# Performance work log

Measured on AMD Instinct MI355X. Metric: run time of the kernel, lower is better.

The kernel has to match this reference:

```python
import jax, jax.numpy as jnp
import numpy as np

N_STEPS = 64          # sample['N']
G = 1.0               # sample['g'] (constant diffusion)
NUM_SAMPLES = 2       # num_samples_per_obs
W_SCALE = 0.05

# interpolant coefficients: alpha(s)=1-s, beta(s)=s, sigma(s)=1-s
# derivatives: alpha_dot=-1, beta_dot=1, sigma_dot=-1

def b_net(x, x0, s, W1, b1, W2, b2, W3, b3):
    # B_net(interpolant, current_state, s): MLP on concat([x, x0, s])
    sf = jnp.full(x.shape[:-1] + (1,), s, dtype=x.dtype)
    inp = jnp.concatenate([x, x0, sf], axis=-1)      # [B, 2*dim+1]
    h = jax.nn.relu(inp @ W1 + b1)
    h = jax.nn.relu(h @ W2 + b2)
    return h @ W3 + b3                                # [B, dim]


def setup_inputs() -> dict:
    key = jax.random.key(0)
    ks = jax.random.split(key, 4)
    num_obs, dim, hid = 65536, 64, 256
    X0 = jax.random.normal(ks[0], (num_obs, dim), dtype=jnp.float32)
    W1 = jax.random.normal(ks[1], (2 * dim + 1, hid), dtype=jnp.float32) * W_SCALE
    W2 = jax.random.normal(ks[2], (hid, hid), dtype=jnp.float32) * W_SCALE
    W3 = jax.random.normal(ks[3], (hid, dim), dtype=jnp.float32) * W_SCALE
    return {
        "X0": X0,
        "W1": W1, "b1": jnp.zeros((hid,), jnp.float32),
        "W2": W2, "b2": jnp.zeros((hid,), jnp.float32),
        "W3": W3, "b3": jnp.zeros((dim,), jnp.float32),
    }


def reference(X0, W1, b1, W2, b2, W3, b3):
    time = jnp.linspace(0.0, 1.0, N_STEPS + 1, dtype=X0.dtype)
    ds = jnp.asarray(1.0 / N_STEPS, X0.dtype)
    sqrt_ds = jnp.sqrt(ds)
    params = (W1, b1, W2, b2, W3, b3)

    def sample_one(key):
        k0, kloop = jax.random.split(key)
        # first Euler step: X = X0 + ds*B(X0,X0,0) + sigma(0)*sqrt(ds)*eta
        eta0 = jax.random.normal(k0, X0.shape, X0.dtype)
        X = X0 + ds * b_net(X0, X0, time[0], *params) + (1.0 - time[0]) * sqrt_ds * eta0

        def step(carry, n):
            X, key = carry
            key, kn = jax.random.split(key)
            s = time[n]
            al, ald = 1.0 - s, -1.0
            bt, btd = s, 1.0
            sg, sgd = 1.0 - s, -1.0
            drift_b = b_net(X, X0, s, *params)
            # score correction (self.score)
            c = btd * X + (bt * ald - btd * al) * X0
            A = 1.0 / (s * sg * (btd * sg - bt * sgd))
            score = A * (bt * drift_b - c)
            # adjusted drift: drift + 0.5*(g^2 - sigma^2)*score
            control = 0.5 * (G ** 2 - sg ** 2) * score
            eta = jax.random.normal(kn, X.shape, X.dtype)
            X = X + ds * (drift_b + control) + G * sqrt_ds * eta
            return (X, key), None

        (X, _), _ = jax.lax.scan(step, (X, kloop), jnp.arange(1, N_STEPS))
        return X

    keys = jax.random.split(jax.random.key(1), NUM_SAMPLES)
    samples = jax.vmap(sample_one)(keys)   # [num_samples, num_obs, dim]
    return samples
```

## Files before the change

kernel.cpp:

```cpp
#include <hip/hip_runtime.h>
#include <stdint.h>


#define PARTITIONABLE 1

namespace {

constexpr int   kObs    = 65536;
constexpr int   kDim    = 64;
constexpr int   kSteps  = 64;
constexpr float kDs     = 1.0f / 64.0f;
constexpr float kSqrtDs = 0.125f;

constexpr int kWeightBytes = 256 * 1024;
constexpr int kKeysOff     = kWeightBytes;
constexpr int kStabOff     = kKeysOff + 1024;

typedef _Float16 f16x8 __attribute__((ext_vector_type(8)));
typedef _Float16 f16x4 __attribute__((ext_vector_type(4)));
typedef float    f32x4 __attribute__((ext_vector_type(4)));

#define MFMA16(a, b, c) __builtin_amdgcn_mfma_f32_16x16x32_f16((a), (b), (c), 0, 0, 0)

__device__ __forceinline__ uint32_t rotl(uint32_t v, int r) {
  return (v << r) | (v >> (32 - r));
}

__device__ __forceinline__ void tf2x32(uint32_t k0, uint32_t k1,
                                       uint32_t& x0, uint32_t& x1) {
  uint32_t k2 = k0 ^ k1 ^ 0x1BD11BDAu;
  x0 += k0; x1 += k1;
  x0 += x1; x1 = rotl(x1, 13); x1 ^= x0;
  x0 += x1; x1 = rotl(x1, 15); x1 ^= x0;
  x0 += x1; x1 = rotl(x1, 26); x1 ^= x0;
  x0 += x1; x1 = rotl(x1,  6); x1 ^= x0;
  x0 += k1; x1 += k2 + 1u;
  x0 += x1; x1 = rotl(x1, 17); x1 ^= x0;
  x0 += x1; x1 = rotl(x1, 29); x1 ^= x0;
  x0 += x1; x1 = rotl(x1, 16); x1 ^= x0;
  x0 += x1; x1 = rotl(x1, 24); x1 ^= x0;
  x0 += k2; x1 += k0 + 2u;
  x0 += x1; x1 = rotl(x1, 13); x1 ^= x0;
  x0 += x1; x1 = rotl(x1, 15); x1 ^= x0;
  x0 += x1; x1 = rotl(x1, 26); x1 ^= x0;
  x0 += x1; x1 = rotl(x1,  6); x1 ^= x0;
  x0 += k0; x1 += k1 + 3u;
  x0 += x1; x1 = rotl(x1, 17); x1 ^= x0;
  x0 += x1; x1 = rotl(x1, 29); x1 ^= x0;
  x0 += x1; x1 = rotl(x1, 16); x1 ^= x0;
  x0 += x1; x1 = rotl(x1, 24); x1 ^= x0;
  x0 += k1; x1 += k2 + 4u;
  x0 += x1; x1 = rotl(x1, 13); x1 ^= x0;
  x0 += x1; x1 = rotl(x1, 15); x1 ^= x0;
  x0 += x1; x1 = rotl(x1, 26); x1 ^= x0;
  x0 += x1; x1 = rotl(x1,  6); x1 ^= x0;
  x0 += k2; x1 += k0 + 5u;
}

__device__ __forceinline__ void jax_split(uint32_t k0, uint32_t k1,
                                          uint32_t& a0, uint32_t& a1,
                                          uint32_t& b0, uint32_t& b1) {
#if PARTITIONABLE
  uint32_t x0 = 0u, x1 = 0u; tf2x32(k0, k1, x0, x1); a0 = x0; a1 = x1;
  uint32_t y0 = 0u, y1 = 1u; tf2x32(k0, k1, y0, y1); b0 = y0; b1 = y1;
#else
  uint32_t x0 = 0u, x1 = 2u; tf2x32(k0, k1, x0, x1);
  uint32_t y0 = 1u, y1 = 3u; tf2x32(k0, k1, y0, y1);
  a0 = x0; a1 = y0; b0 = x1; b1 = y1;
#endif
}

__device__ __forceinline__ uint32_t draw_bits(uint32_t k0, uint32_t k1, uint32_t i) {
#if PARTITIONABLE
  uint32_t x0 = 0u, x1 = i;
  tf2x32(k0, k1, x0, x1);
  return x0 ^ x1;
#else
  const uint32_t half = (uint32_t)kObs * kDim / 2;
  if (i < half) {
    uint32_t x0 = i, x1 = i + half; tf2x32(k0, k1, x0, x1); return x0;
  } else {
    uint32_t x0 = i - half, x1 = i; tf2x32(k0, k1, x0, x1); return x1;
  }
#endif
}

__device__ __forceinline__ float erfinv32(float x) {
  float w = -__logf(fmaf(-x, x, 1.0f));
  float p;
  if (w < 5.0f) {
    w = w - 2.5f;
    p =            2.81022636e-08f;
    p = fmaf(p, w, 3.43273939e-07f);
    p = fmaf(p, w, -3.5233877e-06f);
    p = fmaf(p, w, -4.39150654e-06f);
    p = fmaf(p, w, 0.00021858087f);
    p = fmaf(p, w, -0.00125372503f);
    p = fmaf(p, w, -0.00417768164f);
    p = fmaf(p, w, 0.246640727f);
    p = fmaf(p, w, 1.50140941f);
  } else {
    w = sqrtf(w) - 3.0f;
    p =            -0.000200214257f;
    p = fmaf(p, w, 0.000100950558f);
    p = fmaf(p, w, 0.00134934322f);
    p = fmaf(p, w, -0.00367342844f);
    p = fmaf(p, w, 0.00573950773f);
    p = fmaf(p, w, -0.0076224613f);
    p = fmaf(p, w, 0.00943887047f);
    p = fmaf(p, w, 1.00167406f);
    p = fmaf(p, w, 2.83297682f);
  }
  return p * x;
}

__device__ __forceinline__ float bits_to_normal(uint32_t bits) {
  const float lo = -0.99999994f;
  float f = __uint_as_float(0x3f800000u | (bits >> 9)) - 1.0f;
  float u = fmaxf(lo, fmaf(f, 2.0f, lo));
  return 1.41421356237f * erfinv32(u);
}

}

__global__ void prep_weights(const float* __restrict__ W1,
                             const float* __restrict__ W2,
                             const float* __restrict__ W3,
                             _Float16* __restrict__ ws) {
  const int G = blockIdx.x;
  const int t = threadIdx.x;

  if (G >= 256) {
    if (t < 2) {
      uint32_t* kout = (uint32_t*)((char*)ws + kKeysOff) + t * 128;
      uint32_t s0a, s0b, s1a, s1b;
      jax_split(0u, 1u, s0a, s0b, s1a, s1b);
      const uint32_t sk0 = t ? s1a : s0a;
      const uint32_t sk1 = t ? s1b : s0b;
      uint32_t kd0, kd1, kl0, kl1;
      jax_split(sk0, sk1, kd0, kd1, kl0, kl1);
      kout[0] = kd0; kout[1] = kd1;
      for (int n = 1; n < kSteps; ++n) {
        uint32_t na, nb, xa, xb;
        jax_split(kl0, kl1, na, nb, xa, xb);
        kl0 = na; kl1 = nb;
        kout[2 * n] = xa; kout[2 * n + 1] = xb;
      }
    }
    if (t < kSteps) {
      const float s  = (float)t * kDs;
      const float sg = 1.0f - s;
      f32x4 v;
      v[0] = s;
      v[1] = (t == 0) ? 0.0f : 1.0f / (s * sg);
      v[2] = 0.5f * (1.0f - sg * sg);
      v[3] = kDs * v[2] * v[1];
      *(f32x4*)((char*)ws + kStabOff + t * 16) = v;
    }
    return;
  }

  const int lane = t >> 2;
  const int j0   = (t & 3) * 2;
  const int w    = G >> 5;
  const int T    = G & 31;
  const int lm   = lane & 15;
  const int kb   = (lane >> 4) << 3;

#pragma unroll
  for (int jj = 0; jj < 2; ++jj) {
    const int j = j0 + jj;
    float v;
    if (T < 8) {
      const int mt = T >> 2, kt = T & 3;
      const int col = w * 32 + mt * 16 + lm;
      const int k   = kt * 32 + kb + j;
      v = W1[k * 256 + col];
    } else if (T < 24) {
      const int u = T - 8;
      const int mt = u >> 3, kt = u & 7;
      const int col = w * 32 + mt * 16 + lm;
      const int k   = kt * 32 + kb + j;
      v = W2[k * 256 + col];
    } else {
      const int kt  = T - 24;
      const int col = (w >> 1) * 16 + lm;
      const int k   = kt * 32 + kb + j;
      v = W3[k * 64 + col];
    }
    ws[(size_t)G * 512 + lane * 8 + j] = (_Float16)v;
  }
}

__global__ __launch_bounds__(512, 2)
void sde_mfma(const float* __restrict__ X0g,
              const float* __restrict__ W1,
              const float* __restrict__ b1,
              const float* __restrict__ b2,
              const float* __restrict__ b3,
              const _Float16* __restrict__ ws,
              float* __restrict__ out) {
  __shared__ alignas(16) char  xAf [8 * 1024];
  __shared__ alignas(16) char  h1f [32 * 1024];
  __shared__ alignas(16) char  h2f [32 * 1024];
  __shared__ alignas(16) float bb  [832];

  const int t    = threadIdx.x;
  const int w    = t >> 6;
  const int l    = t & 63;
  const int lq   = l >> 4;
  const int lm   = l & 15;
  const int samp = blockIdx.x >> 10;
  const int tile = blockIdx.x & 1023;
  const int r0   = tile * 64;
  const int mt3  = w >> 1;
  const int ntb  = (w & 1) * 2;
  const int d0   = mt3 * 16 + lq * 4;

  const int rb  = l * 16;
  const int lo1 = ((lq >> 1) * 16 + lm) * 16 + (lq & 1) * 8;
  const int kt3 = mt3 >> 1;
  const int ln3 = (((mt3 & 1) * 2 + (lq >> 1)) * 16 + lm) * 16 + (lq & 1) * 8;

  if (t < 256) {
    bb[t]       = b1[t];
    bb[256 + t] = W1[128 * 256 + t];
    bb[512 + t] = b2[t];
  } else if (t < 320) {
    bb[768 + (t - 256)] = b3[t - 256];
  }

  {
    const int li = t >> 3;
    const int ci = (t & 7) * 8;
    const float* p = X0g + (size_t)(r0 + li) * kDim + ci;
    const float4 a = *(const float4*)p;
    const float4 b = *(const float4*)(p + 4);
    f16x8 h;
    h[0] = (_Float16)a.x; h[1] = (_Float16)a.y;
    h[2] = (_Float16)a.z; h[3] = (_Float16)a.w;
    h[4] = (_Float16)b.x; h[5] = (_Float16)b.y;
    h[6] = (_Float16)b.z; h[7] = (_Float16)b.w;
    const int fa = ((ci >> 5) * 4 + (li >> 4)) * 1024 +
                   (((ci >> 3) & 3) * 16 + (li & 15)) * 16;
    *(f16x8*)(xAf + fa) = h;
    *(f16x8*)(h1f + fa) = h;
  }

  float xv[2][4];
  f32x4 x0q[2];
#pragma unroll
  for (int ni = 0; ni < 2; ++ni) {
    const int row = (ntb + ni) * 16 + lm;
    x0q[ni] = *(const f32x4*)(X0g + (size_t)(r0 + row) * kDim + d0);
#pragma unroll
    for (int q = 0; q < 4; ++q) xv[ni][q] = x0q[ni][q];
  }
  const uint32_t giA = (uint32_t)((r0 + ntb * 16 + lm) * kDim + d0);
  const uint32_t giB = giA + 16u * kDim;

  const char* pW = (const char*)ws + (size_t)w * 32768 + l * 16;
  f16x8 wL1[2][2], wx0[2][2], wL2[16], wL3[8];
#pragma unroll
  for (int mt = 0; mt < 2; ++mt) {
    wL1[mt][0] = *(const f16x8*)(pW + (mt * 4 + 0) * 1024);
    wL1[mt][1] = *(const f16x8*)(pW + (mt * 4 + 1) * 1024);
    wx0[mt][0] = *(const f16x8*)(pW + (mt * 4 + 2) * 1024);
    wx0[mt][1] = *(const f16x8*)(pW + (mt * 4 + 3) * 1024);
  }
#pragma unroll
  for (int i = 0; i < 16; ++i) wL2[i] = *(const f16x8*)(pW + (8 + i) * 1024);
#pragma unroll
  for (int i = 0; i < 8; ++i)  wL3[i] = *(const f16x8*)(pW + (24 + i) * 1024);

  const uint32_t* keys = (const uint32_t*)((const char*)ws + kKeysOff) + samp * 128;
  const f32x4*    stab = (const f32x4*)((const char*)ws + kStabOff);

  __syncthreads();

  f16x4 pre[4][2];
#pragma unroll
  for (int nt = 0; nt < 4; ++nt) {
    const f16x8 xf0 = *(const f16x8*)(h1f + (0 * 4 + nt) * 1024 + rb);
    const f16x8 xf1 = *(const f16x8*)(h1f + (1 * 4 + nt) * 1024 + rb);
#pragma unroll
    for (int mt = 0; mt < 2; ++mt) {
      f32x4 p = {0.f, 0.f, 0.f, 0.f};
      p = MFMA16(wx0[mt][0], xf0, p);
      p = MFMA16(wx0[mt][1], xf1, p);
      f16x4 ph;
#pragma unroll
      for (int q = 0; q < 4; ++q) ph[q] = (_Float16)p[q];
      pre[nt][mt] = ph;
    }
  }
  __syncthreads();

  float etaA[4], etaB[4];
  {
    const uint32_t ka = keys[0], kb0 = keys[1];
#pragma unroll
    for (int q = 0; q < 4; ++q) etaA[q] = bits_to_normal(draw_bits(ka, kb0, giA + q));
#pragma unroll
    for (int q = 0; q < 4; ++q) etaB[q] = bits_to_normal(draw_bits(ka, kb0, giB + q));
  }

  for (int n = 0; n < kSteps; ++n) {
    const f32x4 st = stab[n];
    const float s = st[0], P = st[3];
    const int np = (n + 1 < kSteps) ? n + 1 : n;
    const uint32_t kna = keys[2 * np], knb = keys[2 * np + 1];

#pragma unroll
    for (int nt = 0; nt < 4; ++nt) {
      const f16x8 bf0 = *(const f16x8*)(xAf + (0 * 4 + nt) * 1024 + rb);
      const f16x8 bf1 = *(const f16x8*)(xAf + (1 * 4 + nt) * 1024 + rb);
#pragma unroll
      for (int mt = 0; mt < 2; ++mt) {
        f32x4 c = {0.f, 0.f, 0.f, 0.f};
        c = MFMA16(wL1[mt][0], bf0, c);
        c = MFMA16(wL1[mt][1], bf1, c);
        const int nb = w * 32 + mt * 16 + lq * 4;
        const f32x4 bq = *(const f32x4*)&bb[nb];
        const f32x4 wq = *(const f32x4*)&bb[256 + nb];
        const f16x4 ph = pre[nt][mt];
        f16x4 o;
#pragma unroll
        for (int q = 0; q < 4; ++q)
          o[q] = (_Float16)fmaxf(c[q] + (float)ph[q] + fmaf(s, wq[q], bq[q]), 0.f);
        *(f16x4*)(h1f + (w * 4 + nt) * 1024 + mt * 512 + lo1) = o;
      }
    }
    __syncthreads();

    float enA[4], enB[4];
#pragma unroll
    for (int ntp = 0; ntp < 2; ++ntp) {
      f32x4 c[2][2];
#pragma unroll
      for (int mt = 0; mt < 2; ++mt)
#pragma unroll
        for (int ni = 0; ni < 2; ++ni)
          c[mt][ni] = (f32x4){0.f, 0.f, 0.f, 0.f};
#pragma unroll
      for (int half = 0; half < 2; ++half) {
        f16x8 bh[2][4];
#pragma unroll
        for (int ni = 0; ni < 2; ++ni)
#pragma unroll
          for (int k4 = 0; k4 < 4; ++k4)
            bh[ni][k4] = *(const f16x8*)
                (h1f + ((half * 4 + k4) * 4 + ntp * 2 + ni) * 1024 + rb);
#pragma unroll
        for (int mt = 0; mt < 2; ++mt)
#pragma unroll
          for (int k4 = 0; k4 < 4; ++k4) {
            const f16x8 aW = wL2[mt * 8 + half * 4 + k4];
            c[mt][0] = MFMA16(aW, bh[0][k4], c[mt][0]);
            c[mt][1] = MFMA16(aW, bh[1][k4], c[mt][1]);
          }
      }
      if (ntp == 0) {
#pragma unroll
        for (int q = 0; q < 4; ++q)
          enA[q] = bits_to_normal(draw_bits(kna, knb, giA + q));
      } else {
#pragma unroll
        for (int q = 0; q < 4; ++q)
          enB[q] = bits_to_normal(draw_bits(kna, knb, giB + q));
      }
#pragma unroll
      for (int mt = 0; mt < 2; ++mt) {
        const int nb = w * 32 + mt * 16 + lq * 4;
        const f32x4 bq = *(const f32x4*)&bb[512 + nb];
#pragma unroll
        for (int ni = 0; ni < 2; ++ni) {
          f16x4 o;
#pragma unroll
          for (int q = 0; q < 4; ++q)
            o[q] = (_Float16)fmaxf(c[mt][ni][q] + bq[q], 0.f);
          *(f16x4*)(h2f + (w * 4 + ntp * 2 + ni) * 1024 + mt * 512 + lo1) = o;
        }
      }
    }
    __syncthreads();

    const f32x4 b3q = *(const f32x4*)&bb[768 + d0];
#pragma unroll
    for (int ni = 0; ni < 2; ++ni) {
      f32x4 dA = {0.f, 0.f, 0.f, 0.f}, dB = {0.f, 0.f, 0.f, 0.f};
#pragma unroll
      for (int half = 0; half < 2; ++half) {
        f16x8 bh[4];
#pragma unroll
        for (int k4 = 0; k4 < 4; ++k4)
          bh[k4] = *(const f16x8*)
              (h2f + ((half * 4 + k4) * 4 + ntb + ni) * 1024 + rb);
        dA = MFMA16(wL3[half * 4 + 0], bh[0], dA);
        dB = MFMA16(wL3[half * 4 + 1], bh[1], dB);
        dA = MFMA16(wL3[half * 4 + 2], bh[2], dA);
        dB = MFMA16(wL3[half * 4 + 3], bh[3], dB);
      }
      f16x4 hx;
#pragma unroll
      for (int q = 0; q < 4; ++q) {
        const float ov  = dA[q] + dB[q] + b3q[q];
        const float eta = ni ? etaB[q] : etaA[q];
        const float t1  = fmaf(s, ov, x0q[ni][q] - xv[ni][q]);
        float nx = fmaf(kSqrtDs, eta, xv[ni][q]);
        nx = fmaf(kDs, ov, nx);
        nx = fmaf(P, t1, nx);
        xv[ni][q] = nx;
        hx[q] = (_Float16)nx;
      }
      *(f16x4*)(xAf + (kt3 * 4 + ntb + ni) * 1024 + ln3) = hx;
    }
#pragma unroll
    for (int q = 0; q < 4; ++q) { etaA[q] = enA[q]; etaB[q] = enB[q]; }
    __syncthreads();
  }

#pragma unroll
  for (int ni = 0; ni < 2; ++ni) {
    const int row = (ntb + ni) * 16 + lm;
    const size_t ob = (size_t)samp * ((size_t)kObs * kDim) +
                      (size_t)(r0 + row) * kDim + d0;
    f32x4 v;
#pragma unroll
    for (int q = 0; q < 4; ++q) v[q] = xv[ni][q];
    *(f32x4*)(out + ob) = v;
  }
}

extern "C" void kernel_launch(void* const* d_in, const int* in_sizes, int n_in,
                              void* d_out, int out_size, void* d_ws, size_t ws_size,
                              hipStream_t stream) {
  const float* X0 = (const float*)d_in[0];
  const float* W1 = (const float*)d_in[1];
  const float* b1 = (const float*)d_in[2];
  const float* W2 = (const float*)d_in[3];
  const float* b2 = (const float*)d_in[4];
  const float* W3 = (const float*)d_in[5];
  const float* b3 = (const float*)d_in[6];
  _Float16* ws = (_Float16*)d_ws;

  prep_weights<<<dim3(257), dim3(256), 0, stream>>>(W1, W2, W3, ws);
  sde_mfma<<<dim3(2048), dim3(512), 0, stream>>>(X0, W1, b1, b2, b3, ws,
                                                 (float*)d_out);
}
```

Before: 2.798 ms.

## Software-pipeline MLP layers across two row halves within each SDE step

Measured after the change: 2.830 ms. About the same (+1.1%).

```diff
diff --git a/kernel.cpp b/kernel.cpp
--- a/kernel.cpp
+++ b/kernel.cpp
@@ -85,31 +85,31 @@
 #endif
 }
 
-__device__ __forceinline__ float erfinv32(float x) {
+__device__ __forceinline__ float erfinv32s(float x) {
   float w = -__logf(fmaf(-x, x, 1.0f));
   float p;
   if (w < 5.0f) {
     w = w - 2.5f;
-    p =            2.81022636e-08f;
-    p = fmaf(p, w, 3.43273939e-07f);
-    p = fmaf(p, w, -3.5233877e-06f);
-    p = fmaf(p, w, -4.39150654e-06f);
-    p = fmaf(p, w, 0.00021858087f);
-    p = fmaf(p, w, -0.00125372503f);
-    p = fmaf(p, w, -0.00417768164f);
-    p = fmaf(p, w, 0.246640727f);
-    p = fmaf(p, w, 1.50140941f);
+    p =            3.974239e-08f;
+    p = fmaf(p, w, 4.854653e-07f);
+    p = fmaf(p, w, -4.982823e-06f);
+    p = fmaf(p, w, -6.210533e-06f);
+    p = fmaf(p, w, 3.091202e-04f);
+    p = fmaf(p, w, -1.773035e-03f);
+    p = fmaf(p, w, -5.908134e-03f);
+    p = fmaf(p, w, 3.488027e-01f);
+    p = fmaf(p, w, 2.1233135f);
   } else {
     w = sqrtf(w) - 3.0f;
-    p =            -0.000200214257f;
-    p = fmaf(p, w, 0.000100950558f);
-    p = fmaf(p, w, 0.00134934322f);
-    p = fmaf(p, w, -0.00367342844f);
-    p = fmaf(p, w, 0.00573950773f);
-    p = fmaf(p, w, -0.0076224613f);
-    p = fmaf(p, w, 0.00943887047f);
-    p = fmaf(p, w, 1.00167406f);
-    p = fmaf(p, w, 2.83297682f);
+    p =            -2.8314694e-04f;
+    p = fmaf(p, w, 1.4276561e-04f);
+    p = fmaf(p, w, 1.908261e-03f);
+    p = fmaf(p, w, -5.1950111e-03f);
+    p = fmaf(p, w, 8.1168903e-03f);
+    p = fmaf(p, w, -1.07797888e-02f);
+    p = fmaf(p, w, 1.33485780e-02f);
+    p = fmaf(p, w, 1.4165811f);
+    p = fmaf(p, w, 4.0064343f);
   }
   return p * x;
 }
@@ -118,7 +118,7 @@
   const float lo = -0.99999994f;
   float f = __uint_as_float(0x3f800000u | (bits >> 9)) - 1.0f;
   float u = fmaxf(lo, fmaf(f, 2.0f, lo));
-  return 1.41421356237f * erfinv32(u);
+  return erfinv32s(u);
 }
 
 }
@@ -214,7 +214,7 @@
   const int tile = blockIdx.x & 1023;
   const int r0   = tile * 64;
   const int mt3  = w >> 1;
-  const int ntb  = (w & 1) * 2;
+  const int rpar = w & 1;
   const int d0   = mt3 * 16 + lq * 4;
 
   const int rb  = l * 16;
@@ -250,14 +250,14 @@
   float xv[2][4];
   f32x4 x0q[2];
 #pragma unroll
-  for (int ni = 0; ni < 2; ++ni) {
-    const int row = (ntb + ni) * 16 + lm;
-    x0q[ni] = *(const f32x4*)(X0g + (size_t)(r0 + row) * kDim + d0);
-#pragma unroll
-    for (int q = 0; q < 4; ++q) xv[ni][q] = x0q[ni][q];
-  }
-  const uint32_t giA = (uint32_t)((r0 + ntb * 16 + lm) * kDim + d0);
-  const uint32_t giB = giA + 16u * kDim;
+  for (int h = 0; h < 2; ++h) {
+    const int row = (2 * h + rpar) * 16 + lm;
+    x0q[h] = *(const f32x4*)(X0g + (size_t)(r0 + row) * kDim + d0);
+#pragma unroll
+    for (int q = 0; q < 4; ++q) xv[h][q] = x0q[h][q];
+  }
+  const uint32_t giH0 = (uint32_t)((r0 + rpar * 16 + lm) * kDim + d0);
+  const uint32_t giH1 = giH0 + 32u * kDim;
 
   const char* pW = (const char*)ws + (size_t)w * 32768 + l * 16;
   f16x8 wL1[2][2], wx0[2][2], wL2[16], wL3[8];
@@ -296,23 +296,10 @@
   }
   __syncthreads();
 
-  float etaA[4], etaB[4];
-  {
-    const uint32_t ka = keys[0], kb0 = keys[1];
-#pragma unroll
-    for (int q = 0; q < 4; ++q) etaA[q] = bits_to_normal(draw_bits(ka, kb0, giA + q));
-#pragma unroll
-    for (int q = 0; q < 4; ++q) etaB[q] = bits_to_normal(draw_bits(ka, kb0, giB + q));
-  }
-
-  for (int n = 0; n < kSteps; ++n) {
-    const f32x4 st = stab[n];
-    const float s = st[0], P = st[3];
-    const int np = (n + 1 < kSteps) ? n + 1 : n;
-    const uint32_t kna = keys[2 * np], knb = keys[2 * np + 1];
-
-#pragma unroll
-    for (int nt = 0; nt < 4; ++nt) {
+  auto L1C = [&](int h, float sv) {
+#pragma unroll
+    for (int j = 0; j < 2; ++j) {
+      const int nt = 2 * h + j;
       const f16x8 bf0 = *(const f16x8*)(xAf + (0 * 4 + nt) * 1024 + rb);
       const f16x8 bf1 = *(const f16x8*)(xAf + (1 * 4 + nt) * 1024 + rb);
 #pragma unroll
@@ -327,107 +314,117 @@
         f16x4 o;
 #pragma unroll
         for (int q = 0; q < 4; ++q)
-          o[q] = (_Float16)fmaxf(c[q] + (float)ph[q] + fmaf(s, wq[q], bq[q]), 0.f);
+          o[q] = (_Float16)fmaxf(c[q] + (float)ph[q] + fmaf(sv, wq[q], bq[q]), 0.f);
         *(f16x4*)(h1f + (w * 4 + nt) * 1024 + mt * 512 + lo1) = o;
       }
     }
+  };
+
+  auto L2C = [&](int h) {
+    f32x4 c[2][2];
+#pragma unroll
+    for (int mt = 0; mt < 2; ++mt)
+#pragma unroll
+      for (int ni = 0; ni < 2; ++ni)
+        c[mt][ni] = (f32x4){0.f, 0.f, 0.f, 0.f};
+#pragma unroll
+    for (int kh = 0; kh < 2; ++kh) {
+      f16x8 bh[2][4];
+#pragma unroll
+      for (int ni = 0; ni < 2; ++ni)
+#pragma unroll
+        for (int k4 = 0; k4 < 4; ++k4)
+          bh[ni][k4] = *(const f16x8*)
+              (h1f + ((kh * 4 + k4) * 4 + 2 * h + ni) * 1024 + rb);
+#pragma unroll
+      for (int mt = 0; mt < 2; ++mt)
+#pragma unroll
+        for (int k4 = 0; k4 < 4; ++k4) {
+          const f16x8 aW = wL2[mt * 8 + kh * 4 + k4];
+          c[mt][0] = MFMA16(aW, bh[0][k4], c[mt][0]);
+          c[mt][1] = MFMA16(aW, bh[1][k4], c[mt][1]);
+        }
+    }
+#pragma unroll
+    for (int mt = 0; mt < 2; ++mt) {
+      const int nb = w * 32 + mt * 16 + lq * 4;
+      const f32x4 bq = *(const f32x4*)&bb[512 + nb];
+#pragma unroll
+      for (int ni = 0; ni < 2; ++ni) {
+        f16x4 o;
+#pragma unroll
+        for (int q = 0; q < 4; ++q)
+          o[q] = (_Float16)fmaxf(c[mt][ni][q] + bq[q], 0.f);
+        *(f16x4*)(h2f + (w * 4 + 2 * h + ni) * 1024 + mt * 512 + lo1) = o;
+      }
+    }
+  };
+
+  auto L3U = [&](int h, const float* eta, float sv, float Pv) {
+    const int rt = 2 * h + rpar;
+    f32x4 dA = {0.f, 0.f, 0.f, 0.f}, dB = {0.f, 0.f, 0.f, 0.f};
+#pragma unroll
+    for (int kh = 0; kh < 2; ++kh) {
+      f16x8 bh[4];
+#pragma unroll
+      for (int k4 = 0; k4 < 4; ++k4)
+        bh[k4] = *(const f16x8*)(h2f + ((kh * 4 + k4) * 4 + rt) * 1024 + rb);
+      dA = MFMA16(wL3[kh * 4 + 0], bh[0], dA);
+      dB = MFMA16(wL3[kh * 4 + 1], bh[1], dB);
+      dA = MFMA16(wL3[kh * 4 + 2], bh[2], dA);
+      dB = MFMA16(wL3[kh * 4 + 3], bh[3], dB);
+    }
+    const f32x4 b3q = *(const f32x4*)&bb[768 + d0];
+    f16x4 hx;
+#pragma unroll
+    for (int q = 0; q < 4; ++q) {
+      const float ov = dA[q] + dB[q] + b3q[q];
+      const float t1 = fmaf(sv, ov, x0q[h][q] - xv[h][q]);
+      float nx = fmaf(kSqrtDs, eta[q], xv[h][q]);
+      nx = fmaf(kDs, ov, nx);
+      nx = fmaf(Pv, t1, nx);
+      xv[h][q] = nx;
+      hx[q] = (_Float16)nx;
+    }
+    *(f16x4*)(xAf + (kt3 * 4 + rt) * 1024 + ln3) = hx;
+  };
+
+  L1C(0, stab[0][0]);
+  __syncthreads();
+
+  float et0[4], et1[4];
+  for (int n = 0; n < kSteps; ++n) {
+    const f32x4 st = stab[n];
+    const float s = st[0], P = st[3];
+    const uint32_t ka = keys[2 * n], kb = keys[2 * n + 1];
+
+    L2C(0);
+    L1C(1, s);
+#pragma unroll
+    for (int q = 0; q < 4; ++q)
+      et0[q] = bits_to_normal(draw_bits(ka, kb, giH0 + q));
     __syncthreads();
 
-    float enA[4], enB[4];
-#pragma unroll
-    for (int ntp = 0; ntp < 2; ++ntp) {
-      f32x4 c[2][2];
-#pragma unroll
-      for (int mt = 0; mt < 2; ++mt)
-#pragma unroll
-        for (int ni = 0; ni < 2; ++ni)
-          c[mt][ni] = (f32x4){0.f, 0.f, 0.f, 0.f};
-#pragma unroll
-      for (int half = 0; half < 2; ++half) {
-        f16x8 bh[2][4];
-#pragma unroll
-        for (int ni = 0; ni < 2; ++ni)
-#pragma unroll
-          for (int k4 = 0; k4 < 4; ++k4)
-            bh[ni][k4] = *(const f16x8*)
-                (h1f + ((half * 4 + k4) * 4 + ntp * 2 + ni) * 1024 + rb);
-#pragma unroll
-        for (int mt = 0; mt < 2; ++mt)
-#pragma unroll
-          for (int k4 = 0; k4 < 4; ++k4) {
-            const f16x8 aW = wL2[mt * 8 + half * 4 + k4];
-            c[mt][0] = MFMA16(aW, bh[0][k4], c[mt][0]);
-            c[mt][1] = MFMA16(aW, bh[1][k4], c[mt][1]);
-          }
-      }
-      if (ntp == 0) {
-#pragma unroll
-        for (int q = 0; q < 4; ++q)
-          enA[q] = bits_to_normal(draw_bits(kna, knb, giA + q));
-      } else {
-#pragma unroll
-        for (int q = 0; q < 4; ++q)
-          enB[q] = bits_to_normal(draw_bits(kna, knb, giB + q));
-      }
-#pragma unroll
-      for (int mt = 0; mt < 2; ++mt) {
-        const int nb = w * 32 + mt * 16 + lq * 4;
-        const f32x4 bq = *(const f32x4*)&bb[512 + nb];
-#pragma unroll
-        for (int ni = 0; ni < 2; ++ni) {
-          f16x4 o;
-#pragma unroll
-          for (int q = 0; q < 4; ++q)
-            o[q] = (_Float16)fmaxf(c[mt][ni][q] + bq[q], 0.f);
-          *(f16x4*)(h2f + (w * 4 + ntp * 2 + ni) * 1024 + mt * 512 + lo1) = o;
-        }
-      }
-    }
+    L2C(1);
+    L3U(0, et0, s, P);
+#pragma unroll
+    for (int q = 0; q < 4; ++q)
+      et1[q] = bits_to_normal(draw_bits(ka, kb, giH1 + q));
     __syncthreads();
 
-    const f32x4 b3q = *(const f32x4*)&bb[768 + d0];
-#pragma unroll
-    for (int ni = 0; ni < 2; ++ni) {
-      f32x4 dA = {0.f, 0.f, 0.f, 0.f}, dB = {0.f, 0.f, 0.f, 0.f};
-#pragma unroll
-      for (int half = 0; half < 2; ++half) {
-        f16x8 bh[4];
-#pragma unroll
-        for (int k4 = 0; k4 < 4; ++k4)
-          bh[k4] = *(const f16x8*)
-              (h2f + ((half * 4 + k4) * 4 + ntb + ni) * 1024 + rb);
-        dA = MFMA16(wL3[half * 4 + 0], bh[0], dA);
-        dB = MFMA16(wL3[half * 4 + 1], bh[1], dB);
-        dA = MFMA16(wL3[half * 4 + 2], bh[2], dA);
-        dB = MFMA16(wL3[half * 4 + 3], bh[3], dB);
-      }
-      f16x4 hx;
-#pragma unroll
-      for (int q = 0; q < 4; ++q) {
-        const float ov  = dA[q] + dB[q] + b3q[q];
-        const float eta = ni ? etaB[q] : etaA[q];
-        const float t1  = fmaf(s, ov, x0q[ni][q] - xv[ni][q]);
-        float nx = fmaf(kSqrtDs, eta, xv[ni][q]);
-        nx = fmaf(kDs, ov, nx);
-        nx = fmaf(P, t1, nx);
-        xv[ni][q] = nx;
-        hx[q] = (_Float16)nx;
-      }
-      *(f16x4*)(xAf + (kt3 * 4 + ntb + ni) * 1024 + ln3) = hx;
-    }
-#pragma unroll
-    for (int q = 0; q < 4; ++q) { etaA[q] = enA[q]; etaB[q] = enB[q]; }
+    if (n + 1 < kSteps) L1C(0, stab[n + 1][0]);
+    L3U(1, et1, s, P);
     __syncthreads();
   }
 
 #pragma unroll
-  for (int ni = 0; ni < 2; ++ni) {
-    const int row = (ntb + ni) * 16 + lm;
+  for (int h = 0; h < 2; ++h) {
+    const int row = (2 * h + rpar) * 16 + lm;
     const size_t ob = (size_t)samp * ((size_t)kObs * kDim) +
                       (size_t)(r0 + row) * kDim + d0;
     f32x4 v;
 #pragma unroll
-    for (int q = 0; q < 4; ++q) v[q] = xv[ni][q];
+    for (int q = 0; q < 4; ++q) v[q] = xv[h][q];
     *(f32x4*)(out + ob) = v;
   }
 }
```

## Swizzle LDS fragment layout, hoist biases into registers, fold sqrt2 into erfinv

Applied to the files above, without the earlier changes.

Measured after the change: 3.111 ms. 1.11x slower.

```diff
diff --git a/kernel.cpp b/kernel.cpp
--- a/kernel.cpp
+++ b/kernel.cpp
@@ -21,6 +21,7 @@
 typedef float    f32x4 __attribute__((ext_vector_type(4)));
 
 #define MFMA16(a, b, c) __builtin_amdgcn_mfma_f32_16x16x32_f16((a), (b), (c), 0, 0, 0)
+#define SWZ(b) ((b) ^ (((b) >> 2) & 0x20))
 
 __device__ __forceinline__ uint32_t rotl(uint32_t v, int r) {
   return (v << r) | (v >> (32 - r));
@@ -85,31 +86,31 @@
 #endif
 }
 
-__device__ __forceinline__ float erfinv32(float x) {
+__device__ __forceinline__ float erfinv32s(float x) {
   float w = -__logf(fmaf(-x, x, 1.0f));
   float p;
   if (w < 5.0f) {
     w = w - 2.5f;
-    p =            2.81022636e-08f;
-    p = fmaf(p, w, 3.43273939e-07f);
-    p = fmaf(p, w, -3.5233877e-06f);
-    p = fmaf(p, w, -4.39150654e-06f);
-    p = fmaf(p, w, 0.00021858087f);
-    p = fmaf(p, w, -0.00125372503f);
-    p = fmaf(p, w, -0.00417768164f);
-    p = fmaf(p, w, 0.246640727f);
-    p = fmaf(p, w, 1.50140941f);
+    p =            3.974239e-08f;
+    p = fmaf(p, w, 4.854653e-07f);
+    p = fmaf(p, w, -4.982823e-06f);
+    p = fmaf(p, w, -6.210533e-06f);
+    p = fmaf(p, w, 3.091202e-04f);
+    p = fmaf(p, w, -1.773035e-03f);
+    p = fmaf(p, w, -5.908134e-03f);
+    p = fmaf(p, w, 3.488027e-01f);
+    p = fmaf(p, w, 2.1233135f);
   } else {
     w = sqrtf(w) - 3.0f;
-    p =            -0.000200214257f;
-    p = fmaf(p, w, 0.000100950558f);
-    p = fmaf(p, w, 0.00134934322f);
-    p = fmaf(p, w, -0.00367342844f);
-    p = fmaf(p, w, 0.00573950773f);
-    p = fmaf(p, w, -0.0076224613f);
-    p = fmaf(p, w, 0.00943887047f);
-    p = fmaf(p, w, 1.00167406f);
-    p = fmaf(p, w, 2.83297682f);
+    p =            -2.8314694e-04f;
+    p = fmaf(p, w, 1.4276561e-04f);
+    p = fmaf(p, w, 1.908261e-03f);
+    p = fmaf(p, w, -5.1950111e-03f);
+    p = fmaf(p, w, 8.1168903e-03f);
+    p = fmaf(p, w, -1.07797888e-02f);
+    p = fmaf(p, w, 1.33485780e-02f);
+    p = fmaf(p, w, 1.4165811f);
+    p = fmaf(p, w, 4.0064343f);
   }
   return p * x;
 }
@@ -118,7 +119,7 @@
   const float lo = -0.99999994f;
   float f = __uint_as_float(0x3f800000u | (bits >> 9)) - 1.0f;
   float u = fmaxf(lo, fmaf(f, 2.0f, lo));
-  return 1.41421356237f * erfinv32(u);
+  return erfinv32s(u);
 }
 
 }
@@ -217,10 +218,12 @@
   const int ntb  = (w & 1) * 2;
   const int d0   = mt3 * 16 + lq * 4;
 
-  const int rb  = l * 16;
-  const int lo1 = ((lq >> 1) * 16 + lm) * 16 + (lq & 1) * 8;
-  const int kt3 = mt3 >> 1;
-  const int ln3 = (((mt3 & 1) * 2 + (lq >> 1)) * 16 + lm) * 16 + (lq & 1) * 8;
+  const int rbs  = SWZ(l * 16);
+  const int lo1  = ((lq >> 1) * 16 + lm) * 16 + (lq & 1) * 8;
+  const int lo1s = SWZ(lo1);
+  const int kt3  = mt3 >> 1;
+  const int ln3  = (((mt3 & 1) * 2 + (lq >> 1)) * 16 + lm) * 16 + (lq & 1) * 8;
+  const int ln3s = SWZ(ln3);
 
   if (t < 256) {
     bb[t]       = b1[t];
@@ -241,10 +244,10 @@
     h[2] = (_Float16)a.z; h[3] = (_Float16)a.w;
     h[4] = (_Float16)b.x; h[5] = (_Float16)b.y;
     h[6] = (_Float16)b.z; h[7] = (_Float16)b.w;
-    const int fa = ((ci >> 5) * 4 + (li >> 4)) * 1024 +
-                   (((ci >> 3) & 3) * 16 + (li & 15)) * 16;
-    *(f16x8*)(xAf + fa) = h;
-    *(f16x8*)(h1f + fa) = h;
+    const int fat = ((ci >> 5) * 4 + (li >> 4)) * 1024;
+    const int fai = ((((ci >> 3) & 3) * 16 + (li & 15))) * 16;
+    *(f16x8*)(xAf + fat + SWZ(fai)) = h;
+    *(f16x8*)(h1f + fat + SWZ(fai)) = h;
   }
 
   float xv[2][4];
@@ -278,11 +281,21 @@
 
   __syncthreads();
 
+  f32x4 b1q[2], w1q[2], b2q[2], b3q;
+#pragma unroll
+  for (int mt = 0; mt < 2; ++mt) {
+    const int nb = w * 32 + mt * 16 + lq * 4;
+    b1q[mt] = *(const f32x4*)&bb[nb];
+    w1q[mt] = *(const f32x4*)&bb[256 + nb];
+    b2q[mt] = *(const f32x4*)&bb[512 + nb];
+  }
+  b3q = *(const f32x4*)&bb[768 + d0];
+
   f16x4 pre[4][2];
 #pragma unroll
   for (int nt = 0; nt < 4; ++nt) {
-    const f16x8 xf0 = *(const f16x8*)(h1f + (0 * 4 + nt) * 1024 + rb);
-    const f16x8 xf1 = *(const f16x8*)(h1f + (1 * 4 + nt) * 1024 + rb);
+    const f16x8 xf0 = *(const f16x8*)(h1f + (0 * 4 + nt) * 1024 + rbs);
+    const f16x8 xf1 = *(const f16x8*)(h1f + (1 * 4 + nt) * 1024 + rbs);
 #pragma unroll
     for (int mt = 0; mt < 2; ++mt) {
       f32x4 p = {0.f, 0.f, 0.f, 0.f};
@@ -313,22 +326,22 @@
 
 #pragma unroll
     for (int nt = 0; nt < 4; ++nt) {
-      const f16x8 bf0 = *(const f16x8*)(xAf + (0 * 4 + nt) * 1024 + rb);
-      const f16x8 bf1 = *(const f16x8*)(xAf + (1 * 4 + nt) * 1024 + rb);
+      const f16x8 bf0 = *(const f16x8*)(xAf + (0 * 4 + nt) * 1024 + rbs);
+      const f16x8 bf1 = *(const f16x8*)(xAf + (1 * 4 + nt) * 1024 + rbs);
 #pragma unroll
       for (int mt = 0; mt < 2; ++mt) {
-        f32x4 c = {0.f, 0.f, 0.f, 0.f};
+        const f16x4 ph = pre[nt][mt];
+        f32x4 c;
+#pragma unroll
+        for (int q = 0; q < 4; ++q)
+          c[q] = (float)ph[q] + fmaf(s, w1q[mt][q], b1q[mt][q]);
         c = MFMA16(wL1[mt][0], bf0, c);
         c = MFMA16(wL1[mt][1], bf1, c);
-        const int nb = w * 32 + mt * 16 + lq * 4;
-        const f32x4 bq = *(const f32x4*)&bb[nb];
-        const f32x4 wq = *(const f32x4*)&bb[256 + nb];
-        const f16x4 ph = pre[nt][mt];
         f16x4 o;
 #pragma unroll
         for (int q = 0; q < 4; ++q)
-          o[q] = (_Float16)fmaxf(c[q] + (float)ph[q] + fmaf(s, wq[q], bq[q]), 0.f);
-        *(f16x4*)(h1f + (w * 4 + nt) * 1024 + mt * 512 + lo1) = o;
+          o[q] = (_Float16)fmaxf(c[q], 0.f);
+        *(f16x4*)(h1f + (w * 4 + nt) * 1024 + mt * 512 + lo1s) = o;
       }
     }
     __syncthreads();
@@ -338,10 +351,10 @@
     for (int ntp = 0; ntp < 2; ++ntp) {
       f32x4 c[2][2];
 #pragma unroll
-      for (int mt = 0; mt < 2; ++mt)
-#pragma unroll
-        for (int ni = 0; ni < 2; ++ni)
-          c[mt][ni] = (f32x4){0.f, 0.f, 0.f, 0.f};
+      for (int mt = 0; mt < 2; ++mt) {
+        c[mt][0] = b2q[mt];
+        c[mt][1] = b2q[mt];
+      }
 #pragma unroll
       for (int half = 0; half < 2; ++half) {
         f16x8 bh[2][4];
@@ -350,7 +363,7 @@
 #pragma unroll
           for (int k4 = 0; k4 < 4; ++k4)
             bh[ni][k4] = *(const f16x8*)
-                (h1f + ((half * 4 + k4) * 4 + ntp * 2 + ni) * 1024 + rb);
+                (h1f + ((half * 4 + k4) * 4 + ntp * 2 + ni) * 1024 + rbs);
 #pragma unroll
         for (int mt = 0; mt < 2; ++mt)
 #pragma unroll
@@ -371,31 +384,28 @@
       }
 #pragma unroll
       for (int mt = 0; mt < 2; ++mt) {
-        const int nb = w * 32 + mt * 16 + lq * 4;
-        const f32x4 bq = *(const f32x4*)&bb[512 + nb];
 #pragma unroll
         for (int ni = 0; ni < 2; ++ni) {
           f16x4 o;
 #pragma unroll
           for (int q = 0; q < 4; ++q)
-            o[q] = (_Float16)fmaxf(c[mt][ni][q] + bq[q], 0.f);
-          *(f16x4*)(h2f + (w * 4 + ntp * 2 + ni) * 1024 + mt * 512 + lo1) = o;
+            o[q] = (_Float16)fmaxf(c[mt][ni][q], 0.f);
+          *(f16x4*)(h2f + (w * 4 + ntp * 2 + ni) * 1024 + mt * 512 + lo1s) = o;
         }
       }
     }
     __syncthreads();
 
-    const f32x4 b3q = *(const f32x4*)&bb[768 + d0];
 #pragma unroll
     for (int ni = 0; ni < 2; ++ni) {
-      f32x4 dA = {0.f, 0.f, 0.f, 0.f}, dB = {0.f, 0.f, 0.f, 0.f};
+      f32x4 dA = b3q, dB = {0.f, 0.f, 0.f, 0.f};
 #pragma unroll
       for (int half = 0; half < 2; ++half) {
         f16x8 bh[4];
 #pragma unroll
         for (int k4 = 0; k4 < 4; ++k4)
           bh[k4] = *(const f16x8*)
-              (h2f + ((half * 4 + k4) * 4 + ntb + ni) * 1024 + rb);
+              (h2f + ((half * 4 + k4) * 4 + ntb + ni) * 1024 + rbs);
         dA = MFMA16(wL3[half * 4 + 0], bh[0], dA);
         dB = MFMA16(wL3[half * 4 + 1], bh[1], dB);
         dA = MFMA16(wL3[half * 4 + 2], bh[2], dA);
@@ -404,7 +414,7 @@
       f16x4 hx;
 #pragma unroll
       for (int q = 0; q < 4; ++q) {
-        const float ov  = dA[q] + dB[q] + b3q[q];
+        const float ov  = dA[q] + dB[q];
         const float eta = ni ? etaB[q] : etaA[q];
         const float t1  = fmaf(s, ov, x0q[ni][q] - xv[ni][q]);
         float nx = fmaf(kSqrtDs, eta, xv[ni][q]);
@@ -413,7 +423,7 @@
         xv[ni][q] = nx;
         hx[q] = (_Float16)nx;
       }
-      *(f16x4*)(xAf + (kt3 * 4 + ntb + ni) * 1024 + ln3) = hx;
+      *(f16x4*)(xAf + (kt3 * 4 + ntb + ni) * 1024 + ln3s) = hx;
     }
 #pragma unroll
     for (int q = 0; q < 4; ++q) { etaA[q] = enA[q]; etaB[q] = enB[q]; }
```
